# Kernel optimization log

Measured on AMD Instinct MI355X. Metric: run time of the kernel, lower is better.

Reference implementation:

```python
import jax, jax.numpy as jnp
import numpy as np

B, N, E, V, L, H, FF = 8, 256, 512, 512, 4, 8, 2048
PAD = 0

def _layernorm(x, g, b):
    m = x.mean(-1, keepdims=True)
    v = ((x - m) ** 2).mean(-1, keepdims=True)
    return (x - m) / jnp.sqrt(v + 1e-5) * g + b


def setup_inputs() -> dict:
    key = jax.random.key(0)
    ks = jax.random.split(key, 20)
    s = 0.02
    inp = {
        'src_tokens': jax.random.randint(ks[0], (B, N), 1, V),  # avoid pad id 0
        'padded_coordinates': jax.random.normal(ks[1], (B, N, 3), jnp.float32),
        'src_distance': jax.random.uniform(ks[2], (B, N, N), jnp.float32) * 10.0,
        'src_edge_type': jax.random.randint(ks[3], (B, N, N), 0, 32),
        'embed': (jax.random.normal(ks[4], (V, E), jnp.float32) * s).at[PAD].set(0.0),
        'dp_w1': jax.random.normal(ks[5], (E, 1), jnp.float32) * s,
        'dp_b1': jnp.zeros((E,), jnp.float32),
        'dp_w2': jax.random.normal(ks[6], (1, E), jnp.float32) * s,
        'dp_b2': jnp.zeros((1,), jnp.float32),
        'Wqkv': jax.random.normal(ks[7], (L, 3 * E, E), jnp.float32) * s,
        'bqkv': jnp.zeros((L, 3 * E), jnp.float32),
        'Wo': jax.random.normal(ks[8], (L, E, E), jnp.float32) * s,
        'bo': jnp.zeros((L, E), jnp.float32),
        'ln1_g': jnp.ones((L, E), jnp.float32),
        'ln1_b': jnp.zeros((L, E), jnp.float32),
        'W1': jax.random.normal(ks[9], (L, FF, E), jnp.float32) * s,
        'b1': jnp.zeros((L, FF), jnp.float32),
        'W2': jax.random.normal(ks[10], (L, E, FF), jnp.float32) * s,
        'b2': jnp.zeros((L, E), jnp.float32),
        'ln2_g': jnp.ones((L, E), jnp.float32),
        'ln2_b': jnp.zeros((L, E), jnp.float32),
    }
    return inp


def reference(src_tokens, padded_coordinates, src_distance, src_edge_type,
              embed, dp_w1, dp_b1, dp_w2, dp_b2,
              Wqkv, bqkv, Wo, bo, ln1_g, ln1_b, W1, b1, W2, b2, ln2_g, ln2_b):
    pad_mask = src_tokens == PAD  # [B,N] bool
    x = embed[src_tokens]  # [B,N,E]

    # dist_proj: Linear(1,E) -> tanh -> Linear(E,1) on [B,N,N,1]
    h = jnp.tanh(src_distance[..., None] * dp_w1[:, 0] + dp_b1)  # [B,N,N,E]
    bias = jnp.einsum('bqke,e->bqk', h, dp_w2[0]) + dp_b2[0]      # [B,N,N]
    bias = jnp.where(pad_mask[:, None, :], -jnp.inf, bias)
    bias = jnp.where(pad_mask[:, :, None], -jnp.inf, bias)

    dh = E // H
    scale = 1.0 / jnp.sqrt(jnp.float32(dh))
    nl = Wqkv.shape[0]
    for l in range(nl):
        qkv = x @ Wqkv[l].T + bqkv[l]
        q, k, v = jnp.split(qkv, 3, axis=-1)
        q = q.reshape(B, N, H, dh).transpose(0, 2, 1, 3)
        k = k.reshape(B, N, H, dh).transpose(0, 2, 1, 3)
        v = v.reshape(B, N, H, dh).transpose(0, 2, 1, 3)
        scores = jnp.einsum('bhqd,bhkd->bhqk', q, k) * scale + bias[:, None]
        a = jax.nn.softmax(scores, axis=-1)
        o = jnp.einsum('bhqk,bhkd->bhqd', a, v).transpose(0, 2, 1, 3).reshape(B, N, E)
        x = _layernorm(x + o @ Wo[l].T + bo[l], ln1_g[l], ln1_b[l])
        ff = jax.nn.gelu(x @ W1[l].T + b1[l], approximate=False) @ W2[l].T + b2[l]
        x = _layernorm(x + ff, ln2_g[l], ln2_b[l])
    return x, pad_mask
```

## Files before the change

### kernel.cpp

```cpp
#include <hip/hip_runtime.h>
#include <hip/hip_bf16.h>


namespace {
constexpr int Bn  = 8;
constexpr int Nn  = 256;
constexpr int En  = 512;
constexpr int Ln  = 4;
constexpr int Hn  = 8;
constexpr int FFn = 2048;
constexpr int DHn = 64;
constexpr int Mn  = Bn * Nn;
constexpr int QKV_LD = 3 * En;
constexpr int LUT_N = 4096;
}

typedef float f32x4 __attribute__((ext_vector_type(4)));
typedef short bf16x8 __attribute__((ext_vector_type(8)));

__device__ __forceinline__ unsigned short f2bs(float f) {
    union { float f; unsigned u; } v; v.f = f;
    unsigned r = v.u + 0x7FFFu + ((v.u >> 16) & 1u);
    return (unsigned short)(r >> 16);
}
__device__ __forceinline__ float bf2f(short s) {
    union { unsigned u; float f; } v;
    v.u = ((unsigned)(unsigned short)s) << 16;
    return v.f;
}

__device__ __forceinline__ int swz(int row, int byte_in_row, int stride_b) {
    return row * stride_b + (byte_in_row ^ ((row & 7) << 4));
}

__device__ __forceinline__ void gload_lds16(const void* g, void* l) {
    __builtin_amdgcn_global_load_lds(
        (const __attribute__((address_space(1))) unsigned int*)g,
        (__attribute__((address_space(3))) unsigned int*)l,
        16, 0, 0);
}

struct CvtArgs {
    const float* src[4];
    unsigned short* dst[4];
    int n4[4];
    int blkoff[5];
};
__global__ __launch_bounds__(256) void k_cvt(CvtArgs a) {
    int bid = blockIdx.x;
    int r = 0;
    if (bid >= a.blkoff[1]) r = 1;
    if (bid >= a.blkoff[2]) r = 2;
    if (bid >= a.blkoff[3]) r = 3;
    int i = (bid - a.blkoff[r]) * 256 + threadIdx.x;
    if (i >= a.n4[r]) return;
    f32x4 v = *(const f32x4*)(a.src[r] + (size_t)i * 4);
    unsigned short o[4] = {f2bs(v[0]), f2bs(v[1]), f2bs(v[2]), f2bs(v[3])};
    *(unsigned long long*)(a.dst[r] + (size_t)i * 4) = *(unsigned long long*)o;
}

__global__ __launch_bounds__(256) void k_embed_lut(const int* __restrict__ tok,
                                                   const float* __restrict__ emb,
                                                   float* __restrict__ x,
                                                   unsigned short* __restrict__ xb,
                                                   const float* __restrict__ w1,
                                                   const float* __restrict__ b1,
                                                   const float* __restrict__ w2,
                                                   float* __restrict__ lut) {
    constexpr int EMB_BLOCKS = Mn * En / 256;
    if (blockIdx.x < EMB_BLOCKS) {
        int i = blockIdx.x * 256 + threadIdx.x;
        int m = i >> 9;
        int e = i & 511;
        float v = emb[tok[m] * En + e];
        x[i] = v;
        xb[i] = f2bs(v);
        return;
    }
    __shared__ float sw1[En], sb1[En], sw2[En];
    for (int e = threadIdx.x; e < En; e += 256) {
        sw1[e] = w1[e]; sb1[e] = b1[e]; sw2[e] = w2[e];
    }
    __syncthreads();
    int i = (blockIdx.x - EMB_BLOCKS) * 256 + threadIdx.x;
    if (i > LUT_N) return;
    float d = (float)i * (10.0f / (float)LUT_N);
    float acc = 0.f;
#pragma unroll 4
    for (int e = 0; e < En; ++e) {
        float s = fmaf(d, sw1[e], sb1[e]);
        float t = 1.f - 2.f / (__expf(2.f * s) + 1.f);
        acc = fmaf(t, sw2[e], acc);
    }
    lut[i] = acc;
}

__global__ __launch_bounds__(256) void k_distbias_lut(const float* __restrict__ dist,
                                                      const int* __restrict__ tok,
                                                      const float* __restrict__ lut,
                                                      const float* __restrict__ b2,
                                                      float* __restrict__ biasmat) {
    int i = blockIdx.x * 256 + threadIdx.x;
    float d = dist[i];
    float idx = d * ((float)LUT_N / 10.0f);
    int ii = (int)idx;
    ii = ii < 0 ? 0 : (ii > LUT_N - 1 ? LUT_N - 1 : ii);
    float frac = idx - (float)ii;
    float v0 = lut[ii], v1 = lut[ii + 1];
    float acc = fmaf(v1 - v0, frac, v0) + b2[0];
    int k = i & (Nn - 1);
    int q = (i >> 8) & (Nn - 1);
    int b = i >> 16;
    bool pad = (tok[b * Nn + k] == 0) || (tok[b * Nn + q] == 0);
    biasmat[i] = pad ? -1e30f : acc;
}

__global__ __launch_bounds__(256, 1) void k_attn(
        const unsigned short* __restrict__ qkvb,
        const float* __restrict__ biasmat,
        unsigned short* __restrict__ attnb) {
    __shared__ short Qs[64 * 64];
    __shared__ short Ks[256 * 64];
    __shared__ short Vs[64 * 256];
    __shared__ short Ps[64 * 256];

    const int tid = threadIdx.x;
    const int lane = tid & 63;
    const int wv = tid >> 6;
    const int q0 = blockIdx.x * 64;
    const int bh = blockIdx.y;
    const int b = bh >> 3, h = bh & 7;

    const unsigned short* Qg = qkvb + ((size_t)(b * Nn + q0)) * QKV_LD + h * DHn;
    const unsigned short* Kg = qkvb + ((size_t)(b * Nn)) * QKV_LD + En + h * DHn;
    const unsigned short* VgR = qkvb + ((size_t)(b * Nn)) * QKV_LD + 2 * En + h * DHn;

    {
        const char* src = (const char*)(Kg + (size_t)tid * QKV_LD);
#pragma unroll
        for (int c = 0; c < 8; ++c)
            *(bf16x8*)((char*)Ks + swz(tid, c * 16, 128)) =
                *(const bf16x8*)(src + c * 16);
    }
    {
        const char* src = (const char*)(VgR + (size_t)tid * QKV_LD);
#pragma unroll
        for (int c = 0; c < 8; ++c) {
            bf16x8 v = *(const bf16x8*)(src + c * 16);
#pragma unroll
            for (int j = 0; j < 8; ++j) {
                int d = c * 8 + j;
                *(short*)((char*)Vs + (d * 512 + ((tid * 2) ^ ((d & 7) << 4)))) = v[j];
            }
        }
    }
    {
        int r = tid & 63;
        const char* src = (const char*)(Qg + (size_t)r * QKV_LD);
#pragma unroll
        for (int i = 0; i < 2; ++i) {
            int cb = ((tid >> 6) * 2 + i) * 16;
            bf16x8 v = *(const bf16x8*)(src + cb);
            bf16x8 o;
#pragma unroll
            for (int j = 0; j < 8; ++j) o[j] = (short)f2bs(bf2f(v[j]) * 0.125f);
            *(bf16x8*)((char*)Qs + swz(r, cb, 128)) = o;
        }
    }

    const int qw = wv * 16;
    const int g  = lane >> 4;
    const int c  = lane & 15;
    f32x4 acc[16];
    {
        const float* bb = biasmat + ((size_t)b * Nn + (q0 + qw + g * 4)) * Nn;
#pragma unroll
        for (int f = 0; f < 16; ++f)
#pragma unroll
            for (int r = 0; r < 4; ++r)
                acc[f][r] = bb[(size_t)r * Nn + f * 16 + c];
    }

    __syncthreads();

    bf16x8 qa[2];
#pragma unroll
    for (int ks = 0; ks < 2; ++ks)
        qa[ks] = *(const bf16x8*)((const char*)Qs + swz(qw + c, ks * 64 + g * 16, 128));
#pragma unroll
    for (int f = 0; f < 16; ++f) {
#pragma unroll
        for (int ks = 0; ks < 2; ++ks) {
            bf16x8 kb = *(const bf16x8*)((const char*)Ks +
                         swz(f * 16 + c, ks * 64 + g * 16, 128));
            acc[f] = __builtin_amdgcn_mfma_f32_16x16x32_bf16(qa[ks], kb, acc[f], 0, 0, 0);
        }
    }

    float rcp[4];
#pragma unroll
    for (int r = 0; r < 4; ++r) {
        float m = acc[0][r];
#pragma unroll
        for (int f = 1; f < 16; ++f) m = fmaxf(m, acc[f][r]);
#pragma unroll
        for (int o = 1; o < 16; o <<= 1) m = fmaxf(m, __shfl_xor(m, o));
        float s = 0.f;
#pragma unroll
        for (int f = 0; f < 16; ++f) {
            float e = __expf(acc[f][r] - m);
            acc[f][r] = e;
            s += e;
        }
#pragma unroll
        for (int o = 1; o < 16; o <<= 1) s += __shfl_xor(s, o);
        rcp[r] = 1.f / s;
    }

#pragma unroll
    for (int f = 0; f < 16; ++f)
#pragma unroll
        for (int r = 0; r < 4; ++r) {
            int q = qw + g * 4 + r;
            int kx = f * 16 + c;
            *(unsigned short*)((char*)Ps + (q * 512 + ((kx * 2) ^ ((q & 7) << 4)))) =
                f2bs(acc[f][r] * rcp[r]);
        }

    f32x4 acc2[4];
#pragma unroll
    for (int fd = 0; fd < 4; ++fd) acc2[fd] = {0.f, 0.f, 0.f, 0.f};
#pragma unroll
    for (int ks2 = 0; ks2 < 8; ++ks2) {
        bf16x8 pa = *(const bf16x8*)((const char*)Ps +
                      swz(qw + c, ks2 * 64 + g * 16, 512));
#pragma unroll
        for (int fd = 0; fd < 4; ++fd) {
            bf16x8 vb = *(const bf16x8*)((const char*)Vs +
                          swz(fd * 16 + c, ks2 * 64 + g * 16, 512));
            acc2[fd] = __builtin_amdgcn_mfma_f32_16x16x32_bf16(pa, vb, acc2[fd], 0, 0, 0);
        }
    }

    unsigned short* Cg = attnb + ((size_t)(b * Nn + q0 + qw)) * En + h * DHn;
#pragma unroll
    for (int fd = 0; fd < 4; ++fd)
#pragma unroll
        for (int r = 0; r < 4; ++r)
            Cg[(size_t)(g * 4 + r) * En + fd * 16 + c] = f2bs(acc2[fd][r]);
}

template <int BM, int BN, int BK, int MODE, int CBF>
__global__ __launch_bounds__(256) void k_gemm(
        const unsigned short* __restrict__ A, int lda,
        const unsigned short* __restrict__ Bw, int ldb,
        const float* __restrict__ bias,
        void* __restrict__ Cp, int ldc, long long sCz,
        int K) {
    static_assert(BM == 64 && BN == 64 && BK == 64, "fixed geometry");
    __shared__ short As[2][64 * 64];
    __shared__ short Bs[2][64 * 64];

    const int tid  = threadIdx.x;
    const int lane = tid & 63;
    const int wv   = tid >> 6;
    const int wr   = wv >> 1, wc = wv & 1;
    const int m0 = blockIdx.x * BM, n0 = blockIdx.y * BN;
    const int z  = blockIdx.z;

    const int r_in = lane >> 3;
    const int ch   = lane & 7;
    const size_t koff2 = (size_t)z * K * 2;

    auto stage = [&](int t, int d) {
        const size_t cb = koff2 + (size_t)t * BK * 2;
#pragma unroll
        for (int q = 0; q < 2; ++q) {
            const int rb = q * 32 + wv * 8;
            const char* ga = (const char*)A +
                (size_t)(m0 + rb + r_in) * lda * 2 + cb + ((ch ^ r_in) << 4);
            gload_lds16(ga, &As[d][rb * 64]);
        }
#pragma unroll
        for (int q = 0; q < 2; ++q) {
            const int rb = q * 32 + wv * 8;
            const char* gb = (const char*)Bw +
                (size_t)(n0 + rb + r_in) * ldb * 2 + cb + ((ch ^ r_in) << 4);
            gload_lds16(gb, &Bs[d][rb * 64]);
        }
    };

    f32x4 acc[2][2];
#pragma unroll
    for (int i = 0; i < 2; ++i)
#pragma unroll
        for (int j = 0; j < 2; ++j) acc[i][j] = {0.f, 0.f, 0.f, 0.f};

    const int fkb  = (lane >> 4) * 16;
    const int frow = lane & 15;

    stage(0, 0);
    __syncthreads();

    int cur = 0;
    const int nt = K / BK;
    for (int t = 0; t < nt; ++t) {
        if (t + 1 < nt) stage(t + 1, cur ^ 1);
#pragma unroll
        for (int ks = 0; ks < 2; ++ks) {
            bf16x8 af[2], bfr[2];
#pragma unroll
            for (int i = 0; i < 2; ++i)
                af[i] = *(const bf16x8*)((const char*)As[cur] +
                         swz(wr * 32 + i * 16 + frow, ks * 64 + fkb, 128));
#pragma unroll
            for (int j = 0; j < 2; ++j)
                bfr[j] = *(const bf16x8*)((const char*)Bs[cur] +
                          swz(wc * 32 + j * 16 + frow, ks * 64 + fkb, 128));
#pragma unroll
            for (int i = 0; i < 2; ++i)
#pragma unroll
                for (int j = 0; j < 2; ++j)
                    acc[i][j] = __builtin_amdgcn_mfma_f32_16x16x32_bf16(
                        af[i], bfr[j], acc[i][j], 0, 0, 0);
        }
        __syncthreads();
        cur ^= 1;
    }

#pragma unroll
    for (int i = 0; i < 2; ++i) {
#pragma unroll
        for (int j = 0; j < 2; ++j) {
            const int n = n0 + wc * 32 + j * 16 + (lane & 15);
            float bv = 0.f;
            if constexpr (MODE == 0 || MODE == 1) bv = bias[n];
#pragma unroll
            for (int r = 0; r < 4; ++r) {
                const int m = m0 + wr * 32 + i * 16 + (lane >> 4) * 4 + r;
                float v = acc[i][j][r] + bv;
                if constexpr (MODE == 1)
                    v = 0.5f * v * (1.f + erff(v * 0.70710678118654752f));
                if constexpr (CBF)
                    ((unsigned short*)Cp)[(size_t)m * ldc + n] = f2bs(v);
                else
                    ((float*)Cp)[(size_t)z * sCz + (size_t)m * ldc + n] = v;
            }
        }
    }
}

template <int FINAL>
__global__ __launch_bounds__(256) void k_addln(
        const float* __restrict__ xin,
        const float* __restrict__ yp, long long ystride, int nsplit,
        const float* __restrict__ biasv,
        const float* __restrict__ g, const float* __restrict__ bb,
        float* __restrict__ xout, unsigned short* __restrict__ xbf,
        const int* __restrict__ tok) {
    const int row = blockIdx.x;
    const int tid = threadIdx.x;
    const size_t base = (size_t)row * En;
    float v0 = xin[base + tid] + biasv[tid];
    float v1 = xin[base + tid + 256] + biasv[tid + 256];
    for (int s = 0; s < nsplit; ++s) {
        v0 += yp[(size_t)s * ystride + base + tid];
        v1 += yp[(size_t)s * ystride + base + tid + 256];
    }
    float s1 = v0 + v1;
    float s2 = v0 * v0 + v1 * v1;
#pragma unroll
    for (int o = 32; o; o >>= 1) {
        s1 += __shfl_xor(s1, o);
        s2 += __shfl_xor(s2, o);
    }
    __shared__ float ws1[4], ws2[4];
    int w = tid >> 6;
    if ((tid & 63) == 0) { ws1[w] = s1; ws2[w] = s2; }
    __syncthreads();
    s1 = (ws1[0] + ws1[1]) + (ws1[2] + ws1[3]);
    s2 = (ws2[0] + ws2[1]) + (ws2[2] + ws2[3]);
    const float rE = 1.f / (float)En;
    float mean = s1 * rE;
    float var = s2 * rE - mean * mean;
    float inv = rsqrtf(var + 1e-5f);
    float o0 = (v0 - mean) * inv * g[tid] + bb[tid];
    float o1 = (v1 - mean) * inv * g[tid + 256] + bb[tid + 256];
    xout[base + tid]       = o0;
    xout[base + tid + 256] = o1;
    if constexpr (FINAL) {
        if (tid == 0)
            xout[(size_t)Mn * En + row] = (tok[row] == 0) ? 1.f : 0.f;
    } else {
        xbf[base + tid]       = f2bs(o0);
        xbf[base + tid + 256] = f2bs(o1);
    }
}

extern "C" void kernel_launch(void* const* d_in, const int* in_sizes, int n_in,
                              void* d_out, int out_size, void* d_ws, size_t ws_size,
                              hipStream_t stream) {
    const int*   tok   = (const int*)  d_in[0];
    const float* dist  = (const float*)d_in[2];
    const float* emb   = (const float*)d_in[4];
    const float* dp_w1 = (const float*)d_in[5];
    const float* dp_b1 = (const float*)d_in[6];
    const float* dp_w2 = (const float*)d_in[7];
    const float* dp_b2 = (const float*)d_in[8];
    const float* Wqkv  = (const float*)d_in[9];
    const float* bqkv  = (const float*)d_in[10];
    const float* Wo    = (const float*)d_in[11];
    const float* bo    = (const float*)d_in[12];
    const float* ln1g  = (const float*)d_in[13];
    const float* ln1b  = (const float*)d_in[14];
    const float* W1    = (const float*)d_in[15];
    const float* b1    = (const float*)d_in[16];
    const float* W2    = (const float*)d_in[17];
    const float* b2    = (const float*)d_in[18];
    const float* ln2g  = (const float*)d_in[19];
    const float* ln2b  = (const float*)d_in[20];

    char* p = (char*)d_ws;
    float*          biasmat = (float*)p;          p += (size_t)Bn*Nn*Nn*4;
    float*          x       = (float*)p;          p += (size_t)Mn*En*4;
    unsigned short* xb      = (unsigned short*)p; p += (size_t)Mn*En*2;
    unsigned short* qkvb    = (unsigned short*)p; p += (size_t)Mn*QKV_LD*2;
    unsigned short* Sffb    = (unsigned short*)p; p += (size_t)Mn*FFn*2;
    unsigned short* attnb   = (unsigned short*)p; p += (size_t)Mn*En*2;
    float*          yp      = (float*)p;          p += (size_t)4*Mn*En*4;
    float*          lut     = (float*)p;          p += (size_t)(LUT_N+8)*4;
    unsigned short* wqkvb   = (unsigned short*)p; p += (size_t)Ln*QKV_LD*En*2;
    unsigned short* wob     = (unsigned short*)p; p += (size_t)Ln*En*En*2;
    unsigned short* w1b     = (unsigned short*)p; p += (size_t)Ln*FFn*En*2;
    unsigned short* w2b     = (unsigned short*)p; p += (size_t)Ln*En*FFn*2;

    {
        CvtArgs a;
        a.src[0] = Wqkv; a.dst[0] = wqkvb; a.n4[0] = Ln * QKV_LD * En / 4;
        a.src[1] = Wo;   a.dst[1] = wob;   a.n4[1] = Ln * En * En / 4;
        a.src[2] = W1;   a.dst[2] = w1b;   a.n4[2] = Ln * FFn * En / 4;
        a.src[3] = W2;   a.dst[3] = w2b;   a.n4[3] = Ln * En * FFn / 4;
        a.blkoff[0] = 0;
        for (int i = 0; i < 4; ++i)
            a.blkoff[i + 1] = a.blkoff[i] + (a.n4[i] + 255) / 256;
        k_cvt<<<a.blkoff[4], 256, 0, stream>>>(a);
    }

    k_embed_lut<<<Mn * En / 256 + (LUT_N + 256) / 256, 256, 0, stream>>>(
        tok, emb, x, xb, dp_w1, dp_b1, dp_w2, lut);
    k_distbias_lut<<<Bn * Nn * Nn / 256, 256, 0, stream>>>(dist, tok, lut, dp_b2,
                                                           biasmat);

    const long long yps = (long long)Mn * En;
    for (int l = 0; l < Ln; ++l) {
        const unsigned short* Wqkv_l = wqkvb + (size_t)l * QKV_LD * En;
        const float*          bqkv_l = bqkv  + (size_t)l * QKV_LD;
        const unsigned short* Wo_l   = wob   + (size_t)l * En * En;
        const unsigned short* W1_l   = w1b   + (size_t)l * FFn * En;
        const float*          b1_l   = b1    + (size_t)l * FFn;
        const unsigned short* W2_l   = w2b   + (size_t)l * En * FFn;

        k_gemm<64, 64, 64, 0, 1>
            <<<dim3(Mn / 64, QKV_LD / 64), 256, 0, stream>>>(
            xb, En, Wqkv_l, En, bqkv_l, qkvb, QKV_LD, 0, En);

        k_attn<<<dim3(Nn / 64, Bn * Hn), 256, 0, stream>>>(qkvb, biasmat, attnb);

        k_gemm<64, 64, 64, 3, 0>
            <<<dim3(Mn / 64, En / 64, 2), 256, 0, stream>>>(
            attnb, En, Wo_l, En, nullptr, yp, En, yps, En / 2);
        k_addln<0><<<Mn, 256, 0, stream>>>(x, yp, yps, 2,
                                           bo + (size_t)l * En,
                                           ln1g + (size_t)l * En, ln1b + (size_t)l * En,
                                           x, xb, tok);

        k_gemm<64, 64, 64, 1, 1>
            <<<dim3(Mn / 64, FFn / 64), 256, 0, stream>>>(
            xb, En, W1_l, En, b1_l, Sffb, FFn, 0, En);

        k_gemm<64, 64, 64, 3, 0>
            <<<dim3(Mn / 64, En / 64, 4), 256, 0, stream>>>(
            Sffb, FFn, W2_l, FFn, nullptr, yp, En, yps, FFn / 4);

        if (l < Ln - 1) {
            k_addln<0><<<Mn, 256, 0, stream>>>(x, yp, yps, 4,
                                               b2 + (size_t)l * En,
                                               ln2g + (size_t)l * En, ln2b + (size_t)l * En,
                                               x, xb, tok);
        } else {
            k_addln<1><<<Mn, 256, 0, stream>>>(x, yp, yps, 4,
                                               b2 + (size_t)l * En,
                                               ln2g + (size_t)l * En, ln2b + (size_t)l * En,
                                               (float*)d_out, nullptr, tok);
        }
    }
}
```

Before: 294.1 us.

## Store residual stream, split-K partials and attention bias in bf16

Drops the fp32 residual copy and keeps the hidden state only in bf16. Split-K GEMM partials and the distance bias matrix are also written in bf16 instead of fp32, and addln loads and stores two elements per thread in packed form. This roughly halves the memory traffic of the partial-sum buffers, the bias reads in attention and the layernorm passes. In exchange it loses accuracy, because the residual is rounded to bf16 every layer and the split-K partials are rounded before they are summed.

```diff
diff --git a/kernel.cpp b/kernel.cpp
--- a/kernel.cpp
+++ b/kernel.cpp
@@ -23,9 +23,9 @@
     unsigned r = v.u + 0x7FFFu + ((v.u >> 16) & 1u);
     return (unsigned short)(r >> 16);
 }
-__device__ __forceinline__ float bf2f(short s) {
+__device__ __forceinline__ float bf2f(unsigned short s) {
     union { unsigned u; float f; } v;
-    v.u = ((unsigned)(unsigned short)s) << 16;
+    v.u = ((unsigned)s) << 16;
     return v.f;
 }
 
@@ -61,7 +61,6 @@
 
 __global__ __launch_bounds__(256) void k_embed_lut(const int* __restrict__ tok,
                                                    const float* __restrict__ emb,
-                                                   float* __restrict__ x,
                                                    unsigned short* __restrict__ xb,
                                                    const float* __restrict__ w1,
                                                    const float* __restrict__ b1,
@@ -72,9 +71,7 @@
         int i = blockIdx.x * 256 + threadIdx.x;
         int m = i >> 9;
         int e = i & 511;
-        float v = emb[tok[m] * En + e];
-        x[i] = v;
-        xb[i] = f2bs(v);
+        xb[i] = f2bs(emb[tok[m] * En + e]);
         return;
     }
     __shared__ float sw1[En], sb1[En], sw2[En];
@@ -99,7 +96,7 @@
                                                       const int* __restrict__ tok,
                                                       const float* __restrict__ lut,
                                                       const float* __restrict__ b2,
-                                                      float* __restrict__ biasmat) {
+                                                      unsigned short* __restrict__ biasmat) {
     int i = blockIdx.x * 256 + threadIdx.x;
     float d = dist[i];
     float idx = d * ((float)LUT_N / 10.0f);
@@ -112,12 +109,12 @@
     int q = (i >> 8) & (Nn - 1);
     int b = i >> 16;
     bool pad = (tok[b * Nn + k] == 0) || (tok[b * Nn + q] == 0);
-    biasmat[i] = pad ? -1e30f : acc;
+    biasmat[i] = f2bs(pad ? -1e30f : acc);
 }
 
 __global__ __launch_bounds__(256, 1) void k_attn(
         const unsigned short* __restrict__ qkvb,
-        const float* __restrict__ biasmat,
+        const unsigned short* __restrict__ biasmat,
         unsigned short* __restrict__ attnb) {
     __shared__ short Qs[64 * 64];
     __shared__ short Ks[256 * 64];
@@ -163,7 +160,7 @@
             bf16x8 v = *(const bf16x8*)(src + cb);
             bf16x8 o;
 #pragma unroll
-            for (int j = 0; j < 8; ++j) o[j] = (short)f2bs(bf2f(v[j]) * 0.125f);
+            for (int j = 0; j < 8; ++j) o[j] = (short)f2bs(bf2f((unsigned short)v[j]) * 0.125f);
             *(bf16x8*)((char*)Qs + swz(r, cb, 128)) = o;
         }
     }
@@ -173,12 +170,12 @@
     const int c  = lane & 15;
     f32x4 acc[16];
     {
-        const float* bb = biasmat + ((size_t)b * Nn + (q0 + qw + g * 4)) * Nn;
+        const unsigned short* bb = biasmat + ((size_t)b * Nn + (q0 + qw + g * 4)) * Nn;
 #pragma unroll
         for (int f = 0; f < 16; ++f)
 #pragma unroll
             for (int r = 0; r < 4; ++r)
-                acc[f][r] = bb[(size_t)r * Nn + f * 16 + c];
+                acc[f][r] = bf2f(bb[(size_t)r * Nn + f * 16 + c]);
     }
 
     __syncthreads();
@@ -250,12 +247,12 @@
             Cg[(size_t)(g * 4 + r) * En + fd * 16 + c] = f2bs(acc2[fd][r]);
 }
 
-template <int BM, int BN, int BK, int MODE, int CBF>
+template <int BM, int BN, int BK, int MODE>
 __global__ __launch_bounds__(256) void k_gemm(
         const unsigned short* __restrict__ A, int lda,
         const unsigned short* __restrict__ Bw, int ldb,
         const float* __restrict__ bias,
-        void* __restrict__ Cp, int ldc, long long sCz,
+        unsigned short* __restrict__ Cp, int ldc, long long sCz,
         int K) {
     static_assert(BM == 64 && BN == 64 && BK == 64, "fixed geometry");
     __shared__ short As[2][64 * 64];
@@ -341,10 +338,7 @@
                 float v = acc[i][j][r] + bv;
                 if constexpr (MODE == 1)
                     v = 0.5f * v * (1.f + erff(v * 0.70710678118654752f));
-                if constexpr (CBF)
-                    ((unsigned short*)Cp)[(size_t)m * ldc + n] = f2bs(v);
-                else
-                    ((float*)Cp)[(size_t)z * sCz + (size_t)m * ldc + n] = v;
+                Cp[(size_t)z * sCz + (size_t)m * ldc + n] = f2bs(v);
             }
         }
     }
@@ -352,20 +346,25 @@
 
 template <int FINAL>
 __global__ __launch_bounds__(256) void k_addln(
-        const float* __restrict__ xin,
-        const float* __restrict__ yp, long long ystride, int nsplit,
+        const unsigned short* __restrict__ xin_b,
+        const unsigned short* __restrict__ yp, long long ystride, int nsplit,
         const float* __restrict__ biasv,
         const float* __restrict__ g, const float* __restrict__ bb,
-        float* __restrict__ xout, unsigned short* __restrict__ xbf,
+        unsigned short* __restrict__ xout_b, float* __restrict__ dout,
         const int* __restrict__ tok) {
     const int row = blockIdx.x;
     const int tid = threadIdx.x;
     const size_t base = (size_t)row * En;
-    float v0 = xin[base + tid] + biasv[tid];
-    float v1 = xin[base + tid + 256] + biasv[tid + 256];
+    const int i0 = 2 * tid;
+
+    unsigned xv = *(const unsigned*)(xin_b + base + i0);
+    float2 bv = *(const float2*)(biasv + i0);
+    float v0 = bf2f((unsigned short)(xv & 0xFFFFu)) + bv.x;
+    float v1 = bf2f((unsigned short)(xv >> 16)) + bv.y;
     for (int s = 0; s < nsplit; ++s) {
-        v0 += yp[(size_t)s * ystride + base + tid];
-        v1 += yp[(size_t)s * ystride + base + tid + 256];
+        unsigned pv = *(const unsigned*)(yp + (size_t)s * ystride + base + i0);
+        v0 += bf2f((unsigned short)(pv & 0xFFFFu));
+        v1 += bf2f((unsigned short)(pv >> 16));
     }
     float s1 = v0 + v1;
     float s2 = v0 * v0 + v1 * v1;
@@ -384,16 +383,17 @@
     float mean = s1 * rE;
     float var = s2 * rE - mean * mean;
     float inv = rsqrtf(var + 1e-5f);
-    float o0 = (v0 - mean) * inv * g[tid] + bb[tid];
-    float o1 = (v1 - mean) * inv * g[tid + 256] + bb[tid + 256];
-    xout[base + tid]       = o0;
-    xout[base + tid + 256] = o1;
+    float2 gv = *(const float2*)(g + i0);
+    float2 bbv = *(const float2*)(bb + i0);
+    float o0 = (v0 - mean) * inv * gv.x + bbv.x;
+    float o1 = (v1 - mean) * inv * gv.y + bbv.y;
     if constexpr (FINAL) {
+        *(float2*)(dout + base + i0) = make_float2(o0, o1);
         if (tid == 0)
-            xout[(size_t)Mn * En + row] = (tok[row] == 0) ? 1.f : 0.f;
+            dout[(size_t)Mn * En + row] = (tok[row] == 0) ? 1.f : 0.f;
     } else {
-        xbf[base + tid]       = f2bs(o0);
-        xbf[base + tid + 256] = f2bs(o1);
+        unsigned ov = (unsigned)f2bs(o0) | ((unsigned)f2bs(o1) << 16);
+        *(unsigned*)(xout_b + base + i0) = ov;
     }
 }
 
@@ -421,13 +421,12 @@
     const float* ln2b  = (const float*)d_in[20];
 
     char* p = (char*)d_ws;
-    float*          biasmat = (float*)p;          p += (size_t)Bn*Nn*Nn*4;
-    float*          x       = (float*)p;          p += (size_t)Mn*En*4;
+    unsigned short* biasmat = (unsigned short*)p; p += (size_t)Bn*Nn*Nn*2;
     unsigned short* xb      = (unsigned short*)p; p += (size_t)Mn*En*2;
     unsigned short* qkvb    = (unsigned short*)p; p += (size_t)Mn*QKV_LD*2;
     unsigned short* Sffb    = (unsigned short*)p; p += (size_t)Mn*FFn*2;
     unsigned short* attnb   = (unsigned short*)p; p += (size_t)Mn*En*2;
-    float*          yp      = (float*)p;          p += (size_t)4*Mn*En*4;
+    unsigned short* yp      = (unsigned short*)p; p += (size_t)4*Mn*En*2;
     float*          lut     = (float*)p;          p += (size_t)(LUT_N+8)*4;
     unsigned short* wqkvb   = (unsigned short*)p; p += (size_t)Ln*QKV_LD*En*2;
     unsigned short* wob     = (unsigned short*)p; p += (size_t)Ln*En*En*2;
@@ -447,7 +446,7 @@
     }
 
     k_embed_lut<<<Mn * En / 256 + (LUT_N + 256) / 256, 256, 0, stream>>>(
-        tok, emb, x, xb, dp_w1, dp_b1, dp_w2, lut);
+        tok, emb, xb, dp_w1, dp_b1, dp_w2, lut);
     k_distbias_lut<<<Bn * Nn * Nn / 256, 256, 0, stream>>>(dist, tok, lut, dp_b2,
                                                            biasmat);
 
@@ -460,38 +459,38 @@
         const float*          b1_l   = b1    + (size_t)l * FFn;
         const unsigned short* W2_l   = w2b   + (size_t)l * En * FFn;
 
-        k_gemm<64, 64, 64, 0, 1>
+        k_gemm<64, 64, 64, 0>
             <<<dim3(Mn / 64, QKV_LD / 64), 256, 0, stream>>>(
             xb, En, Wqkv_l, En, bqkv_l, qkvb, QKV_LD, 0, En);
 
         k_attn<<<dim3(Nn / 64, Bn * Hn), 256, 0, stream>>>(qkvb, biasmat, attnb);
 
-        k_gemm<64, 64, 64, 3, 0>
+        k_gemm<64, 64, 64, 3>
             <<<dim3(Mn / 64, En / 64, 2), 256, 0, stream>>>(
             attnb, En, Wo_l, En, nullptr, yp, En, yps, En / 2);
-        k_addln<0><<<Mn, 256, 0, stream>>>(x, yp, yps, 2,
+        k_addln<0><<<Mn, 256, 0, stream>>>(xb, yp, yps, 2,
                                            bo + (size_t)l * En,
                                            ln1g + (size_t)l * En, ln1b + (size_t)l * En,
-                                           x, xb, tok);
-
-        k_gemm<64, 64, 64, 1, 1>
+                                           xb, nullptr, tok);
+
+        k_gemm<64, 64, 64, 1>
             <<<dim3(Mn / 64, FFn / 64), 256, 0, stream>>>(
             xb, En, W1_l, En, b1_l, Sffb, FFn, 0, En);
 
-        k_gemm<64, 64, 64, 3, 0>
+        k_gemm<64, 64, 64, 3>
             <<<dim3(Mn / 64, En / 64, 4), 256, 0, stream>>>(
             Sffb, FFn, W2_l, FFn, nullptr, yp, En, yps, FFn / 4);
 
         if (l < Ln - 1) {
-            k_addln<0><<<Mn, 256, 0, stream>>>(x, yp, yps, 4,
+            k_addln<0><<<Mn, 256, 0, stream>>>(xb, yp, yps, 4,
                                                b2 + (size_t)l * En,
                                                ln2g + (size_t)l * En, ln2b + (size_t)l * En,
-                                               x, xb, tok);
+                                               xb, nullptr, tok);
         } else {
-            k_addln<1><<<Mn, 256, 0, stream>>>(x, yp, yps, 4,
+            k_addln<1><<<Mn, 256, 0, stream>>>(xb, yp, yps, 4,
                                                b2 + (size_t)l * En,
                                                ln2g + (size_t)l * En, ln2b + (size_t)l * En,
-                                               (float*)d_out, nullptr, tok);
-        }
-    }
-}
+                                               nullptr, (float*)d_out, tok);
+        }
+    }
+}
```

Result: faster. 278.1 us (-5.5%).
